# Optimization experiments

Measured on AMD Instinct MI355X. Metric: run time of the kernel, lower is better.

The kernel has to match this reference:

```python
import jax, jax.numpy as jnp
import numpy as np
from jax import lax

B, S, D, NH, K = 4, 2048, 1024, 16, 3
EPS = 1e-6


def custom_layernorm(x, gamma, beta):
    # torch-style: std with ddof=1, eps added to std (not var)
    mean = jnp.mean(x, axis=-1, keepdims=True)
    var = jnp.sum((x - mean) ** 2, axis=-1, keepdims=True) / (x.shape[-1] - 1)
    std = jnp.sqrt(var)
    return gamma * ((x - mean) / (std + EPS)) + beta


def setup_inputs() -> dict:
    key = jax.random.key(0)
    ks = jax.random.split(key, 10)
    s = 1.0 / np.sqrt(D)
    return {
        "x": jax.random.normal(ks[0], (B, S, D), jnp.float32),
        "Wq": jax.random.normal(ks[1], (D, D), jnp.float32) * s,
        "bq": jax.random.normal(ks[2], (D,), jnp.float32) * 0.02,
        "Wk": jax.random.normal(ks[3], (D, D), jnp.float32) * s,
        "Wv": jax.random.normal(ks[4], (D, D), jnp.float32) * s,
        "bv": jax.random.normal(ks[5], (D,), jnp.float32) * 0.02,
        "conv_w": jax.random.normal(ks[6], (D, D // NH, K), jnp.float32) * (1.0 / np.sqrt((D // NH) * K)),
        "conv_b": jax.random.normal(ks[7], (D,), jnp.float32) * 0.02,
        "gamma": jnp.ones((D,), jnp.float32),
        "beta": jnp.zeros((D,), jnp.float32),
        "Wo": jax.random.normal(ks[8], (D, D), jnp.float32) * s,
        "bo": jax.random.normal(ks[9], (D,), jnp.float32) * 0.02,
    }


def reference(x, Wq, bq, Wk, Wv, bv, conv_w, conv_b, gamma, beta, Wo, bo):
    d = x.shape[-1]
    groups = d // conv_w.shape[1]
    pad = conv_w.shape[2] // 2

    q = x @ Wq + bq
    k = x @ Wk  # key has no bias
    v = x @ Wv + bv

    # grouped conv1d over sequence dim (NCW layout)
    xc = jnp.transpose(x, (0, 2, 1))  # [B, D, S]
    conv_out = lax.conv_general_dilated(
        xc, conv_w, window_strides=(1,), padding=[(pad, pad)],
        feature_group_count=groups,
        dimension_numbers=("NCH", "OIH", "NCH"),
    ) + conv_b[None, :, None]
    conv_out = jnp.transpose(conv_out, (0, 2, 1))  # [B, S, D]
    conv_out = custom_layernorm(conv_out, gamma, beta)  # dropout = identity (eval)

    scale = 1.0 / jnp.sqrt(jnp.asarray(d, x.dtype))
    scores = jnp.einsum("bqd,bkd->bqk", q, k) * scale  # [B, S, S]
    attn = jax.nn.softmax(scores, axis=-1)
    attention_out = jnp.einsum("bqk,bkd->bqd", attn, v)

    combined = custom_layernorm(conv_out + attention_out, gamma, beta)
    return combined @ Wo + bo + x
```

## Files before the change

kernel.cpp:

```cpp
#include <hip/hip_runtime.h>
#include <cstdint>


#define DEV __device__ __forceinline__

typedef unsigned short u16;
typedef __attribute__((ext_vector_type(8))) short bf16x8;
typedef __attribute__((ext_vector_type(4))) float f32x4;

static const int Sn = 2048, Dn = 1024;

DEV float bf2f(u16 u) { union { unsigned int i; float f; } w; w.i = ((unsigned int)u) << 16; return w.f; }
DEV u16 f2bf(float f) {
  union { float f; unsigned int i; } w; w.f = f;
  unsigned int x = w.i;
  return (u16)((x + 0x7FFFu + ((x >> 16) & 1u)) >> 16);
}

DEV void gload_lds16(const u16* gsrc, u16* lds_dst) {
  __builtin_amdgcn_global_load_lds(
      (const __attribute__((address_space(1))) void*)gsrc,
      (__attribute__((address_space(3))) void*)lds_dst,
      16, 0, 0);
}

DEV float block_allreduce_sum(float v, float* red, int tid) {
  #pragma unroll
  for (int o = 32; o > 0; o >>= 1) v += __shfl_down(v, o, 64);
  __syncthreads();
  if ((tid & 63) == 0) red[tid >> 6] = v;
  __syncthreads();
  return red[0] + red[1] + red[2] + red[3];
}

DEV float block_allreduce_max(float v, float* red, int tid) {
  #pragma unroll
  for (int o = 32; o > 0; o >>= 1) v = fmaxf(v, __shfl_down(v, o, 64));
  __syncthreads();
  if ((tid & 63) == 0) red[tid >> 6] = v;
  __syncthreads();
  return fmaxf(fmaxf(red[0], red[1]), fmaxf(red[2], red[3]));
}

DEV void ln_row(const u16* __restrict__ a, const u16* __restrict__ b2,
                const float* __restrict__ gamma, const float* __restrict__ beta,
                u16* __restrict__ out, long row, int tid, float* red) {
  long base = row * Dn + tid * 4;
  ushort4 av = *(const ushort4*)&a[base];
  float v0 = bf2f(av.x), v1 = bf2f(av.y), v2 = bf2f(av.z), v3 = bf2f(av.w);
  if (b2) {
    ushort4 bv4 = *(const ushort4*)&b2[base];
    v0 += bf2f(bv4.x); v1 += bf2f(bv4.y); v2 += bf2f(bv4.z); v3 += bf2f(bv4.w);
  }
  float s = block_allreduce_sum(v0 + v1 + v2 + v3, red, tid);
  float mean = s * (1.0f / 1024.0f);
  float d0 = v0 - mean, d1 = v1 - mean, d2 = v2 - mean, d3 = v3 - mean;
  float sq = block_allreduce_sum(d0 * d0 + d1 * d1 + d2 * d2 + d3 * d3, red, tid);
  float inv = 1.0f / (sqrtf(sq * (1.0f / 1023.0f)) + 1e-6f);
  float4 gv = *(const float4*)&gamma[tid * 4];
  float4 bev = *(const float4*)&beta[tid * 4];
  ushort4 o;
  o.x = f2bf(gv.x * d0 * inv + bev.x);
  o.y = f2bf(gv.y * d1 * inv + bev.y);
  o.z = f2bf(gv.z * d2 * inv + bev.z);
  o.w = f2bf(gv.w * d3 * inv + bev.w);
  *(ushort4*)&out[base] = o;
}

__global__ __launch_bounds__(256)
void prep_all(const float* __restrict__ Wq, const float* __restrict__ Wk,
              const float* __restrict__ Wv, const float* __restrict__ Wo,
              u16* __restrict__ wT,
              const float* __restrict__ bq, const float* __restrict__ bv,
              float* __restrict__ qkvb,
              const float* __restrict__ x, u16* __restrict__ xb) {
  __shared__ u16 sm[64][68];
  int blk = blockIdx.x;
  int tid = threadIdx.x;
  if (blk < 1024) {
    int w = blk >> 8, t = blk & 255;
    const float* src = (w == 0) ? Wq : (w == 1) ? Wk : (w == 2) ? Wv : Wo;
    u16* dst = wT + (size_t)w * 1048576u;
    int i0 = (t >> 4) << 6, j0 = (t & 15) << 6;
    int tx = tid & 15, r0 = tid >> 4;
    #pragma unroll
    for (int rr = r0; rr < 64; rr += 16) {
      float4 v = *(const float4*)&src[(long)(i0 + rr) * 1024 + j0 + tx * 4];
      sm[rr][tx*4+0] = f2bf(v.x); sm[rr][tx*4+1] = f2bf(v.y);
      sm[rr][tx*4+2] = f2bf(v.z); sm[rr][tx*4+3] = f2bf(v.w);
    }
    __syncthreads();
    #pragma unroll
    for (int cc = r0; cc < 64; cc += 16) {
      ushort4 o;
      o.x = sm[tx*4+0][cc]; o.y = sm[tx*4+1][cc];
      o.z = sm[tx*4+2][cc]; o.w = sm[tx*4+3][cc];
      *(ushort4*)&dst[(long)(j0 + cc) * 1024 + i0 + tx * 4] = o;
    }
  } else if (blk == 1024) {
    for (int j = tid; j < 3072; j += 256) {
      float v = 0.0f;
      if (j < 1024) v = bq[j];
      else if (j >= 2048) v = bv[j - 2048];
      qkvb[j] = v;
    }
  } else {
    int i = (blk - 1025) * 1024 + tid * 4;
    float4 v = *(const float4*)&x[i];
    ushort4 o;
    o.x = f2bf(v.x); o.y = f2bf(v.y); o.z = f2bf(v.z); o.w = f2bf(v.w);
    *(ushort4*)&xb[i] = o;
  }
}

template<typename CT>
__global__ __launch_bounds__(256, 2)
void gemm_nt(const u16* __restrict__ A, const u16* __restrict__ A2, long Abs, int lda,
             const u16* __restrict__ B, long Bbs, int ldb,
             CT* __restrict__ C, CT* __restrict__ C2, long Cbs, int ldc,
             int zsplit, int K, float scale,
             const float* __restrict__ bias, int bias_bs,
             const float* __restrict__ res, long Rbs, int ldr) {
  __shared__ u16 sA[2][128 * 32];
  __shared__ u16 sB[2][128 * 32];
  int tid = threadIdx.x;
  int lane = tid & 63, wv = tid >> 6;
  int quad = lane >> 4, lm = lane & 15;
  int wr = wv >> 1, wc = wv & 1;
  long m0 = (long)blockIdx.x * 128, n0 = (long)blockIdx.y * 128;
  int z = blockIdx.z;
  if (z >= zsplit) { A = A2 + (long)(z - zsplit) * Abs; C = C2 + (long)(z - zsplit) * Cbs; }
  else             { A = A  + (long)z * Abs;            C = C  + (long)z * Cbs; }
  B += (long)z * Bbs;
  if (res) res += (long)z * Rbs;

  f32x4 acc[4][4] = {};

  int srow = wv * 16 + (lane >> 2);
  int sch = (lane & 3) * 8;
  const u16* Ap = A + (m0 + srow) * (long)lda + sch;
  const u16* Bp = B + (n0 + srow) * (long)ldb + sch;
  const int lofs = wv * 16 * 32;

  for (int k0 = 0; k0 < K; k0 += 64) {
    #pragma unroll
    for (int h = 0; h < 2; h++) {
      int kh = k0 + h * 32;
      gload_lds16(Ap + kh, &sA[h][lofs]);
      gload_lds16(Ap + 64 * (long)lda + kh, &sA[h][lofs + 64 * 32]);
      gload_lds16(Bp + kh, &sB[h][lofs]);
      gload_lds16(Bp + 64 * (long)ldb + kh, &sB[h][lofs + 64 * 32]);
    }
    __syncthreads();
    #pragma unroll
    for (int h = 0; h < 2; h++) {
      bf16x8 af[4], bfr[4];
      #pragma unroll
      for (int mi = 0; mi < 4; mi++)
        af[mi] = *(const bf16x8*)&sA[h][(wr * 64 + mi * 16 + lm) * 32 + quad * 8];
      #pragma unroll
      for (int ni = 0; ni < 4; ni++)
        bfr[ni] = *(const bf16x8*)&sB[h][(wc * 64 + ni * 16 + lm) * 32 + quad * 8];
      #pragma unroll
      for (int mi = 0; mi < 4; mi++)
        #pragma unroll
        for (int ni = 0; ni < 4; ni++)
          acc[mi][ni] = __builtin_amdgcn_mfma_f32_16x16x32_bf16(af[mi], bfr[ni], acc[mi][ni], 0, 0, 0);
    }
    __syncthreads();
  }

  #pragma unroll
  for (int mi = 0; mi < 4; mi++) {
    #pragma unroll
    for (int ni = 0; ni < 4; ni++) {
      int col = (int)n0 + wc * 64 + ni * 16 + lm;
      float bv = bias ? bias[(long)z * bias_bs + col] : 0.0f;
      #pragma unroll
      for (int r = 0; r < 4; r++) {
        long rowg = m0 + wr * 64 + mi * 16 + quad * 4 + r;
        float v = acc[mi][ni][r] * scale + bv;
        if (res) v += res[rowg * (long)ldr + col];
        if constexpr (sizeof(CT) == 2) C[rowg * (long)ldc + col] = f2bf(v);
        else                           C[rowg * (long)ldc + col] = v;
      }
    }
  }
}

__global__ __launch_bounds__(256, 2)
void post_qkv(int ngemm,
              const u16* __restrict__ Qb, const u16* __restrict__ Kb,
              u16* __restrict__ Pd, u16* __restrict__ Pw,
              const u16* __restrict__ Vb, u16* __restrict__ vt) {
  __shared__ u16 smem[2 * 2 * 128 * 32];
  int blk = blockIdx.x;
  int tid = threadIdx.x;
  if (blk < ngemm) {
    u16* sA0 = smem;
    u16* sB0 = smem + 2 * 128 * 32;
    int lane = tid & 63, wv = tid >> 6;
    int quad = lane >> 4, lm = lane & 15;
    int wr = wv >> 1, wc = wv & 1;
    int z = blk >> 8;
    long m0 = (long)(blk & 15) * 128, n0 = (long)((blk >> 4) & 15) * 128;
    const u16* A = Qb + (long)z * Sn * Dn;
    const u16* B = Kb + (long)z * Sn * Dn;
    u16* C = (z < 2) ? Pd + (long)z * Sn * Sn : Pw + (long)(z - 2) * Sn * Sn;

    f32x4 acc[4][4] = {};
    int srow = wv * 16 + (lane >> 2);
    int sch = (lane & 3) * 8;
    const u16* Ap = A + (m0 + srow) * 1024 + sch;
    const u16* Bp = B + (n0 + srow) * 1024 + sch;
    const int lofs = wv * 16 * 32;

    for (int k0 = 0; k0 < 1024; k0 += 64) {
      #pragma unroll
      for (int h = 0; h < 2; h++) {
        int kh = k0 + h * 32;
        gload_lds16(Ap + kh, &sA0[h * 128 * 32 + lofs]);
        gload_lds16(Ap + 64 * 1024 + kh, &sA0[h * 128 * 32 + lofs + 64 * 32]);
        gload_lds16(Bp + kh, &sB0[h * 128 * 32 + lofs]);
        gload_lds16(Bp + 64 * 1024 + kh, &sB0[h * 128 * 32 + lofs + 64 * 32]);
      }
      __syncthreads();
      #pragma unroll
      for (int h = 0; h < 2; h++) {
        bf16x8 af[4], bfr[4];
        #pragma unroll
        for (int mi = 0; mi < 4; mi++)
          af[mi] = *(const bf16x8*)&sA0[h * 128 * 32 + (wr * 64 + mi * 16 + lm) * 32 + quad * 8];
        #pragma unroll
        for (int ni = 0; ni < 4; ni++)
          bfr[ni] = *(const bf16x8*)&sB0[h * 128 * 32 + (wc * 64 + ni * 16 + lm) * 32 + quad * 8];
        #pragma unroll
        for (int mi = 0; mi < 4; mi++)
          #pragma unroll
          for (int ni = 0; ni < 4; ni++)
            acc[mi][ni] = __builtin_amdgcn_mfma_f32_16x16x32_bf16(af[mi], bfr[ni], acc[mi][ni], 0, 0, 0);
      }
      __syncthreads();
    }
    #pragma unroll
    for (int mi = 0; mi < 4; mi++) {
      #pragma unroll
      for (int ni = 0; ni < 4; ni++) {
        int col = (int)n0 + wc * 64 + ni * 16 + lm;
        #pragma unroll
        for (int r = 0; r < 4; r++) {
          long rowg = m0 + wr * 64 + mi * 16 + quad * 4 + r;
          C[rowg * 2048 + col] = f2bf(acc[mi][ni][r] * 0.03125f);
        }
      }
    }
  } else {
    u16 (*sm)[68] = (u16(*)[68])smem;
    int t = blk - ngemm;
    int b = t >> 9, r = t & 511;
    int j0 = (r & 15) << 6, i0 = ((r >> 4) & 31) << 6;
    const u16* s = Vb + (long)b * Sn * Dn;
    u16* d = vt + (long)b * Dn * Sn;
    int tx = tid & 15, r0 = tid >> 4;
    #pragma unroll
    for (int rr = r0; rr < 64; rr += 16) {
      ushort4 v = *(const ushort4*)&s[(long)(i0 + rr) * 1024 + j0 + tx * 4];
      sm[rr][tx*4+0] = v.x; sm[rr][tx*4+1] = v.y; sm[rr][tx*4+2] = v.z; sm[rr][tx*4+3] = v.w;
    }
    __syncthreads();
    #pragma unroll
    for (int cc = r0; cc < 64; cc += 16) {
      ushort4 o;
      o.x = sm[tx*4+0][cc]; o.y = sm[tx*4+1][cc];
      o.z = sm[tx*4+2][cc]; o.w = sm[tx*4+3][cc];
      *(ushort4*)&d[(long)(j0 + cc) * 2048 + i0 + tx * 4] = o;
    }
  }
}

__global__ __launch_bounds__(256)
void smax_conv(u16* __restrict__ pa, u16* __restrict__ pb, int rowsplit, int nsm,
               const float* __restrict__ x, const float* __restrict__ cw,
               const float* __restrict__ cb, u16* __restrict__ convo) {
  __shared__ u16 smem[22160];
  __shared__ float red[4];
  int blk = blockIdx.x;
  int tid = threadIdx.x;
  if (blk < nsm) {
    long row = blk;
    u16* p = (row < rowsplit) ? pa + row * 2048 : pb + (row - rowsplit) * 2048;
    ushort4 a = *(const ushort4*)&p[tid * 8];
    ushort4 b = *(const ushort4*)&p[tid * 8 + 4];
    float f0 = bf2f(a.x), f1 = bf2f(a.y), f2 = bf2f(a.z), f3 = bf2f(a.w);
    float f4 = bf2f(b.x), f5 = bf2f(b.y), f6 = bf2f(b.z), f7 = bf2f(b.w);
    float m = fmaxf(fmaxf(fmaxf(f0, f1), fmaxf(f2, f3)),
                    fmaxf(fmaxf(f4, f5), fmaxf(f6, f7)));
    m = block_allreduce_max(m, red, tid);
    float e0 = __expf(f0 - m), e1 = __expf(f1 - m), e2 = __expf(f2 - m), e3 = __expf(f3 - m);
    float e4 = __expf(f4 - m), e5 = __expf(f5 - m), e6 = __expf(f6 - m), e7 = __expf(f7 - m);
    float s = block_allreduce_sum(e0 + e1 + e2 + e3 + e4 + e5 + e6 + e7, red, tid);
    float inv = 1.0f / s;
    ushort4 o1, o2;
    o1.x = f2bf(e0 * inv); o1.y = f2bf(e1 * inv); o1.z = f2bf(e2 * inv); o1.w = f2bf(e3 * inv);
    o2.x = f2bf(e4 * inv); o2.y = f2bf(e5 * inv); o2.z = f2bf(e6 * inv); o2.w = f2bf(e7 * inv);
    *(ushort4*)&p[tid * 8] = o1;
    *(ushort4*)&p[tid * 8 + 4] = o2;
  } else {
    u16 (*sx)[72] = (u16(*)[72])smem;
    u16 (*sw)[200] = (u16(*)[200])(smem + 9360);
    int r = blk - nsm;
    int s0 = (r & 15) * 128;
    int g = (r >> 4) & 15;
    int b = r >> 8;
    int lane = tid & 63, wv = tid >> 6;
    int quad = lane >> 4, lm = lane & 15;
    for (int idx = tid; idx < 64 * 192; idx += 256) {
      int oc = idx / 192, k = idx - oc * 192;
      int t = k >> 6, i = k & 63;
      sw[oc][k] = f2bf(cw[((long)(g * 64 + oc)) * 192 + i * 3 + t]);
    }
    for (int idx = tid; idx < 130 * 16; idx += 256) {
      int rr = idx >> 4, c4 = (idx & 15) * 4;
      int s = s0 - 1 + rr;
      ushort4 v;
      if (s >= 0 && s < Sn) {
        float4 f = *(const float4*)&x[((long)b * Sn + s) * Dn + g * 64 + c4];
        v.x = f2bf(f.x); v.y = f2bf(f.y); v.z = f2bf(f.z); v.w = f2bf(f.w);
      } else { v.x = 0; v.y = 0; v.z = 0; v.w = 0; }
      *(ushort4*)&sx[rr][c4] = v;
    }
    __syncthreads();
    f32x4 acc[2][4] = {};
    #pragma unroll
    for (int ks = 0; ks < 6; ks++) {
      int t = ks >> 1;
      int i0 = (ks & 1) * 32 + quad * 8;
      bf16x8 a0 = *(const bf16x8*)&sx[wv * 32 + lm + t][i0];
      bf16x8 a1 = *(const bf16x8*)&sx[wv * 32 + 16 + lm + t][i0];
      #pragma unroll
      for (int nf = 0; nf < 4; nf++) {
        bf16x8 bf = *(const bf16x8*)&sw[nf * 16 + lm][ks * 32 + quad * 8];
        acc[0][nf] = __builtin_amdgcn_mfma_f32_16x16x32_bf16(a0, bf, acc[0][nf], 0, 0, 0);
        acc[1][nf] = __builtin_amdgcn_mfma_f32_16x16x32_bf16(a1, bf, acc[1][nf], 0, 0, 0);
      }
    }
    #pragma unroll
    for (int mi = 0; mi < 2; mi++) {
      #pragma unroll
      for (int nf = 0; nf < 4; nf++) {
        int col = g * 64 + nf * 16 + lm;
        float bias = cb[col];
        #pragma unroll
        for (int rr = 0; rr < 4; rr++) {
          int row = wv * 32 + mi * 16 + quad * 4 + rr;
          convo[((long)b * Sn + s0 + row) * Dn + col] = f2bf(acc[mi][nf][rr] + bias);
        }
      }
    }
  }
}

__global__ __launch_bounds__(256, 2)
void pv_ln(int npv,
           const u16* __restrict__ Pd, const u16* __restrict__ Pw,
           const u16* __restrict__ vt, u16* __restrict__ attn,
           u16* __restrict__ conv,
           const float* __restrict__ gamma, const float* __restrict__ beta) {
  __shared__ u16 smem[2 * 2 * 128 * 32];
  __shared__ float red[4];
  int blk = blockIdx.x;
  int tid = threadIdx.x;
  if (blk < npv) {
    u16* sA0 = smem;
    u16* sB0 = smem + 2 * 128 * 32;
    int lane = tid & 63, wv = tid >> 6;
    int quad = lane >> 4, lm = lane & 15;
    int wr = wv >> 1, wc = wv & 1;
    int z = blk >> 7;
    long m0 = (long)(blk & 15) * 128, n0 = (long)((blk >> 4) & 7) * 128;
    const u16* A = (z < 2) ? Pd + (long)z * Sn * Sn : Pw + (long)(z - 2) * Sn * Sn;
    const u16* B = vt + (long)z * Dn * Sn;
    u16* C = attn + (long)z * Sn * Dn;

    f32x4 acc[4][4] = {};
    int srow = wv * 16 + (lane >> 2);
    int sch = (lane & 3) * 8;
    const u16* Ap = A + (m0 + srow) * 2048 + sch;
    const u16* Bp = B + (n0 + srow) * 2048 + sch;
    const int lofs = wv * 16 * 32;

    for (int k0 = 0; k0 < 2048; k0 += 64) {
      #pragma unroll
      for (int h = 0; h < 2; h++) {
        int kh = k0 + h * 32;
        gload_lds16(Ap + kh, &sA0[h * 128 * 32 + lofs]);
        gload_lds16(Ap + 64 * 2048 + kh, &sA0[h * 128 * 32 + lofs + 64 * 32]);
        gload_lds16(Bp + kh, &sB0[h * 128 * 32 + lofs]);
        gload_lds16(Bp + 64 * 2048 + kh, &sB0[h * 128 * 32 + lofs + 64 * 32]);
      }
      __syncthreads();
      #pragma unroll
      for (int h = 0; h < 2; h++) {
        bf16x8 af[4], bfr[4];
        #pragma unroll
        for (int mi = 0; mi < 4; mi++)
          af[mi] = *(const bf16x8*)&sA0[h * 128 * 32 + (wr * 64 + mi * 16 + lm) * 32 + quad * 8];
        #pragma unroll
        for (int ni = 0; ni < 4; ni++)
          bfr[ni] = *(const bf16x8*)&sB0[h * 128 * 32 + (wc * 64 + ni * 16 + lm) * 32 + quad * 8];
        #pragma unroll
        for (int mi = 0; mi < 4; mi++)
          #pragma unroll
          for (int ni = 0; ni < 4; ni++)
            acc[mi][ni] = __builtin_amdgcn_mfma_f32_16x16x32_bf16(af[mi], bfr[ni], acc[mi][ni], 0, 0, 0);
      }
      __syncthreads();
    }
    #pragma unroll
    for (int mi = 0; mi < 4; mi++) {
      #pragma unroll
      for (int ni = 0; ni < 4; ni++) {
        int col = (int)n0 + wc * 64 + ni * 16 + lm;
        #pragma unroll
        for (int r = 0; r < 4; r++) {
          long rowg = m0 + wr * 64 + mi * 16 + quad * 4 + r;
          C[rowg * 1024 + col] = f2bf(acc[mi][ni][r]);
        }
      }
    }
  } else {
    long row = blk - npv;
    ln_row(conv, nullptr, gamma, beta, conv, row, tid, red);
  }
}

__global__ __launch_bounds__(256)
void ln_kernel(const u16* __restrict__ a, const u16* __restrict__ b2,
               const float* __restrict__ gamma, const float* __restrict__ beta,
               u16* __restrict__ out) {
  __shared__ float red[4];
  ln_row(a, b2, gamma, beta, out, blockIdx.x, threadIdx.x, red);
}

static const size_t OFF_WT    = 0;
static const size_t OFF_QKVB  = 8ull << 20;
static const size_t OFF_Q     = 9ull << 20;
static const size_t OFF_K     = 25ull << 20;
static const size_t OFF_V     = 41ull << 20;
static const size_t OFF_PW    = 57ull << 20;

extern "C" void kernel_launch(void* const* d_in, const int* in_sizes, int n_in,
                              void* d_out, int out_size, void* d_ws, size_t ws_size,
                              hipStream_t stream) {
  const float* x     = (const float*)d_in[0];
  const float* Wq    = (const float*)d_in[1];
  const float* bq    = (const float*)d_in[2];
  const float* Wk    = (const float*)d_in[3];
  const float* Wv    = (const float*)d_in[4];
  const float* bv    = (const float*)d_in[5];
  const float* cw    = (const float*)d_in[6];
  const float* cb    = (const float*)d_in[7];
  const float* gamma = (const float*)d_in[8];
  const float* beta  = (const float*)d_in[9];
  const float* Wo    = (const float*)d_in[10];
  const float* bo    = (const float*)d_in[11];
  float* out = (float*)d_out;
  char* ws = (char*)d_ws;

  u16*   wT    = (u16*)(ws + OFF_WT);
  float* qkvb  = (float*)(ws + OFF_QKVB);
  u16*   Qb    = (u16*)(ws + OFF_Q);
  u16*   Kb    = (u16*)(ws + OFF_K);
  u16*   Vb    = (u16*)(ws + OFF_V);
  u16*   Pw    = (u16*)(ws + OFF_PW);
  u16*   xb    = (u16*)d_out;
  u16*   Pd    = (u16*)d_out;
  u16*   vt    = (u16*)d_out + 8388608;
  u16*   conv  = Vb;
  u16*   attn  = Qb;
  u16*   combined = Kb;
  const long PBS = (long)Sn * Sn;

  dim3 tb(256);

  prep_all<<<dim3(9217), tb, 0, stream>>>(Wq, Wk, Wv, Wo, wT, bq, bv, qkvb, x, xb);
  gemm_nt<u16><<<dim3(64, 8, 3), tb, 0, stream>>>(
      xb, nullptr, 0, 1024, wT, 1048576, 1024, Qb, (u16*)nullptr, 8388608, 1024,
      99, 1024, 1.0f, qkvb, 1024, nullptr, 0, 0);

  if (ws_size >= (73ull << 20)) {
    post_qkv<<<dim3(1024 + 2048), tb, 0, stream>>>(1024, Qb, Kb, Pd, Pw, Vb, vt);
    smax_conv<<<dim3(8192 + 1024), tb, 0, stream>>>(Pd, Pw, 4096, 8192,
                                                    x, cw, cb, conv);
    pv_ln<<<dim3(512 + 8192), tb, 0, stream>>>(512, Pd, Pw, vt, attn, conv,
                                               gamma, beta);
  } else {
    post_qkv<<<dim3(2048), tb, 0, stream>>>(0, Qb, Kb, Pd, Pw, Vb, vt);
    for (int c = 0; c < 2; c++) {
      long off = (long)c * 2 * Sn * Dn;
      gemm_nt<u16><<<dim3(16, 16, 2), tb, 0, stream>>>(
          Qb + off, nullptr, (long)Sn * Dn, 1024, Kb + off, (long)Sn * Dn, 1024,
          Pd, (u16*)nullptr, PBS, 2048,
          99, 1024, 0.03125f, nullptr, 0, nullptr, 0, 0);
      smax_conv<<<dim3(4096 + (c == 0 ? 1024 : 0)), tb, 0, stream>>>(
          Pd, Pd, 4096, 4096, x, cw, cb, conv);
      gemm_nt<u16><<<dim3(16, 8, 2), tb, 0, stream>>>(
          Pd, nullptr, PBS, 2048, vt + off, (long)Dn * Sn, 2048,
          attn + off, (u16*)nullptr, (long)Sn * Dn, 1024,
          99, 2048, 1.0f, nullptr, 0, nullptr, 0, 0);
    }
    ln_kernel<<<dim3(8192), tb, 0, stream>>>(conv, nullptr, gamma, beta, conv);
  }

  ln_kernel<<<dim3(8192), tb, 0, stream>>>(conv, attn, gamma, beta, combined);
  gemm_nt<float><<<dim3(64, 8, 1), tb, 0, stream>>>(
      combined, nullptr, 0, 1024, wT + 3u * 1048576u, 0, 1024,
      out, (float*)nullptr, 0, 1024,
      99, 1024, 1.0f, bo, 0, x, 0, 1024);
}
```

Baseline: 354.0 us.

## Add 256x256 eight-wave GEMM for QKV and QK^T, fold V transpose into softmax

Adds a new 512-thread GEMM kernel with 256x256 tiles, 128KB dynamic LDS double buffering, swizzled direct-to-LDS loads and interleaved barrier/setprio scheduling. It is used for the QKV projection and, in the large-workspace path, for the QK^T score GEMM, which replaces post_qkv. The V transpose moves into extra blocks of the softmax/conv kernel, and conv output is relocated to Kb. The larger tiles are meant to improve data reuse and MFMA utilisation, at the cost of lower occupancy and fewer blocks per launch.

```diff
diff --git a/kernel.cpp b/kernel.cpp
--- a/kernel.cpp
+++ b/kernel.cpp
@@ -111,6 +111,161 @@
     o.x = f2bf(v.x); o.y = f2bf(v.y); o.z = f2bf(v.z); o.w = f2bf(v.w);
     *(ushort4*)&xb[i] = o;
   }
+}
+
+__global__ __launch_bounds__(512, 2)
+void gemm8(const u16* __restrict__ A, long Abs, int lda,
+           const u16* __restrict__ B, long Bbs, int ldb,
+           u16* __restrict__ C0, u16* __restrict__ C1, int zsplit,
+           long Cbs, int ldc, int K, float scale,
+           const float* __restrict__ bias, int bias_bs) {
+  extern __shared__ u16 lds[];
+  int tid = threadIdx.x;
+  int w = tid >> 6, ln = tid & 63;
+  int quad = ln >> 4, lm = ln & 15;
+  int wr = w >> 2, wc = w & 3;
+  long m0 = (long)blockIdx.x * 256, n0 = (long)blockIdx.y * 256;
+  int z = blockIdx.z;
+  A += (long)z * Abs;
+  B += (long)z * Bbs;
+  u16* C = (z < zsplit) ? C0 + (long)z * Cbs : C1 + (long)(z - zsplit) * Cbs;
+
+  int sg = ((ln & 7) ^ (ln >> 3)) * 8;
+  int row0 = w * 8 + (ln >> 3);
+  const u16* As0 = A + (m0 + row0) * (long)lda + sg;
+  const u16* As1 = As0 + 64 * (long)lda;
+  const u16* Bs0 = B + (n0 + row0) * (long)ldb + sg;
+  const u16* Bs1 = Bs0 + 64 * (long)ldb;
+  u16* dA = lds + w * 512;
+  u16* dB = lds + 16384 + w * 512;
+
+  int rA = wr * 16 + lm;
+  int rB = wc * 16 + lm;
+  int g0 = (quad ^ (lm & 7)) * 8;
+  int g1 = ((4 + quad) ^ (lm & 7)) * 8;
+
+#define STGA(buf, h, k0) do { \
+    gload_lds16(As0 + (long)(h) * 128 * lda + (k0), dA + (buf) * 32768 + (h) * 8192); \
+    gload_lds16(As1 + (long)(h) * 128 * lda + (k0), dA + (buf) * 32768 + (h) * 8192 + 4096); } while (0)
+#define STGB(buf, h, k0) do { \
+    gload_lds16(Bs0 + (long)(h) * 128 * ldb + (k0), dB + (buf) * 32768 + (h) * 8192); \
+    gload_lds16(Bs1 + (long)(h) * 128 * ldb + (k0), dB + (buf) * 32768 + (h) * 8192 + 4096); } while (0)
+#define LDA_F(ab, mi, kk) (*(const bf16x8*)&lds[(ab) + ((mi) * 32 + rA) * 64 + ((kk) ? g1 : g0)])
+#define LDB_F(bb, ni, kk) (*(const bf16x8*)&lds[(bb) + ((ni) * 64 + rB) * 64 + ((kk) ? g1 : g0)])
+#define MFMA(a, b, c) __builtin_amdgcn_mfma_f32_16x16x32_bf16(a, b, c, 0, 0, 0)
+
+  f32x4 acc[8][4] = {};
+  bf16x8 bfr[4][2];
+  int nt = K >> 6;
+
+  STGB(0, 0, 0); STGB(0, 1, 0); STGA(0, 0, 0); STGA(0, 1, 0);
+  asm volatile("s_waitcnt vmcnt(2)" ::: "memory");
+  __builtin_amdgcn_sched_barrier(0);
+  __builtin_amdgcn_s_barrier();
+
+  for (int t = 0; t < nt; ++t) {
+    int buf = t & 1;
+    int abase = buf * 32768, bbase = abase + 16384;
+    int nbuf = buf ^ 1;
+    int kn = (t + 1) << 6;
+    bool more = (t + 1 < nt);
+
+    {
+      #pragma unroll
+      for (int ni = 0; ni < 4; ni++) {
+        bfr[ni][0] = LDB_F(bbase, ni, 0);
+        bfr[ni][1] = LDB_F(bbase, ni, 1);
+      }
+      bf16x8 a00 = LDA_F(abase, 0, 0), a01 = LDA_F(abase, 0, 1);
+      bf16x8 a10 = LDA_F(abase, 1, 0), a11 = LDA_F(abase, 1, 1);
+      if (more) STGB(nbuf, 0, kn);
+      __builtin_amdgcn_s_barrier();
+      __builtin_amdgcn_s_setprio(1);
+      #pragma unroll
+      for (int ni = 0; ni < 4; ni++) {
+        acc[0][ni] = MFMA(a00, bfr[ni][0], acc[0][ni]);
+        acc[0][ni] = MFMA(a01, bfr[ni][1], acc[0][ni]);
+        acc[1][ni] = MFMA(a10, bfr[ni][0], acc[1][ni]);
+        acc[1][ni] = MFMA(a11, bfr[ni][1], acc[1][ni]);
+      }
+      __builtin_amdgcn_s_setprio(0);
+      __builtin_amdgcn_s_barrier();
+    }
+    {
+      bf16x8 a00 = LDA_F(abase, 2, 0), a01 = LDA_F(abase, 2, 1);
+      bf16x8 a10 = LDA_F(abase, 3, 0), a11 = LDA_F(abase, 3, 1);
+      if (more) STGB(nbuf, 1, kn);
+      __builtin_amdgcn_s_barrier();
+      __builtin_amdgcn_s_setprio(1);
+      #pragma unroll
+      for (int ni = 0; ni < 4; ni++) {
+        acc[2][ni] = MFMA(a00, bfr[ni][0], acc[2][ni]);
+        acc[2][ni] = MFMA(a01, bfr[ni][1], acc[2][ni]);
+        acc[3][ni] = MFMA(a10, bfr[ni][0], acc[3][ni]);
+        acc[3][ni] = MFMA(a11, bfr[ni][1], acc[3][ni]);
+      }
+      __builtin_amdgcn_s_setprio(0);
+      if (more) asm volatile("s_waitcnt vmcnt(4)" ::: "memory");
+      else      asm volatile("s_waitcnt vmcnt(0)" ::: "memory");
+      __builtin_amdgcn_sched_barrier(0);
+      __builtin_amdgcn_s_barrier();
+    }
+    {
+      bf16x8 a00 = LDA_F(abase, 4, 0), a01 = LDA_F(abase, 4, 1);
+      bf16x8 a10 = LDA_F(abase, 5, 0), a11 = LDA_F(abase, 5, 1);
+      if (more) STGA(nbuf, 0, kn);
+      __builtin_amdgcn_s_barrier();
+      __builtin_amdgcn_s_setprio(1);
+      #pragma unroll
+      for (int ni = 0; ni < 4; ni++) {
+        acc[4][ni] = MFMA(a00, bfr[ni][0], acc[4][ni]);
+        acc[4][ni] = MFMA(a01, bfr[ni][1], acc[4][ni]);
+        acc[5][ni] = MFMA(a10, bfr[ni][0], acc[5][ni]);
+        acc[5][ni] = MFMA(a11, bfr[ni][1], acc[5][ni]);
+      }
+      __builtin_amdgcn_s_setprio(0);
+      __builtin_amdgcn_s_barrier();
+    }
+    {
+      bf16x8 a00 = LDA_F(abase, 6, 0), a01 = LDA_F(abase, 6, 1);
+      bf16x8 a10 = LDA_F(abase, 7, 0), a11 = LDA_F(abase, 7, 1);
+      if (more) STGA(nbuf, 1, kn);
+      __builtin_amdgcn_s_barrier();
+      __builtin_amdgcn_s_setprio(1);
+      #pragma unroll
+      for (int ni = 0; ni < 4; ni++) {
+        acc[6][ni] = MFMA(a00, bfr[ni][0], acc[6][ni]);
+        acc[6][ni] = MFMA(a01, bfr[ni][1], acc[6][ni]);
+        acc[7][ni] = MFMA(a10, bfr[ni][0], acc[7][ni]);
+        acc[7][ni] = MFMA(a11, bfr[ni][1], acc[7][ni]);
+      }
+      __builtin_amdgcn_s_setprio(0);
+      if (more) {
+        asm volatile("s_waitcnt vmcnt(2)" ::: "memory");
+        __builtin_amdgcn_sched_barrier(0);
+      }
+      __builtin_amdgcn_s_barrier();
+    }
+  }
+
+  #pragma unroll
+  for (int mi = 0; mi < 8; mi++) {
+    #pragma unroll
+    for (int ni = 0; ni < 4; ni++) {
+      int col = (int)n0 + ni * 64 + wc * 16 + lm;
+      float bvv = bias ? bias[(long)z * bias_bs + col] : 0.0f;
+      #pragma unroll
+      for (int r = 0; r < 4; r++) {
+        long rowg = m0 + mi * 32 + wr * 16 + quad * 4 + r;
+        C[rowg * (long)ldc + col] = f2bf(acc[mi][ni][r] * scale + bvv);
+      }
+    }
+  }
+#undef STGA
+#undef STGB
+#undef LDA_F
+#undef LDB_F
+#undef MFMA
 }
 
 template<typename CT>
@@ -279,9 +434,11 @@
 }
 
 __global__ __launch_bounds__(256)
-void smax_conv(u16* __restrict__ pa, u16* __restrict__ pb, int rowsplit, int nsm,
+void smax_conv(u16* __restrict__ pa, u16* __restrict__ pb, int rowsplit,
+               int nsm, int nconv,
                const float* __restrict__ x, const float* __restrict__ cw,
-               const float* __restrict__ cb, u16* __restrict__ convo) {
+               const float* __restrict__ cb, u16* __restrict__ convo,
+               const u16* __restrict__ Vb, u16* __restrict__ vt) {
   __shared__ u16 smem[22160];
   __shared__ float red[4];
   int blk = blockIdx.x;
@@ -305,7 +462,7 @@
     o2.x = f2bf(e4 * inv); o2.y = f2bf(e5 * inv); o2.z = f2bf(e6 * inv); o2.w = f2bf(e7 * inv);
     *(ushort4*)&p[tid * 8] = o1;
     *(ushort4*)&p[tid * 8 + 4] = o2;
-  } else {
+  } else if (blk < nsm + nconv) {
     u16 (*sx)[72] = (u16(*)[72])smem;
     u16 (*sw)[200] = (u16(*)[200])(smem + 9360);
     int r = blk - nsm;
@@ -356,6 +513,27 @@
           convo[((long)b * Sn + s0 + row) * Dn + col] = f2bf(acc[mi][nf][rr] + bias);
         }
       }
+    }
+  } else {
+    u16 (*sm)[68] = (u16(*)[68])smem;
+    int t = blk - nsm - nconv;
+    int b = t >> 9, r = t & 511;
+    int j0 = (r & 15) << 6, i0 = ((r >> 4) & 31) << 6;
+    const u16* s = Vb + (long)b * Sn * Dn;
+    u16* d = vt + (long)b * Dn * Sn;
+    int tx = tid & 15, r0 = tid >> 4;
+    #pragma unroll
+    for (int rr = r0; rr < 64; rr += 16) {
+      ushort4 v = *(const ushort4*)&s[(long)(i0 + rr) * 1024 + j0 + tx * 4];
+      sm[rr][tx*4+0] = v.x; sm[rr][tx*4+1] = v.y; sm[rr][tx*4+2] = v.z; sm[rr][tx*4+3] = v.w;
+    }
+    __syncthreads();
+    #pragma unroll
+    for (int cc = r0; cc < 64; cc += 16) {
+      ushort4 o;
+      o.x = sm[tx*4+0][cc]; o.y = sm[tx*4+1][cc];
+      o.z = sm[tx*4+2][cc]; o.w = sm[tx*4+3][cc];
+      *(ushort4*)&d[(long)(j0 + cc) * 2048 + i0 + tx * 4] = o;
     }
   }
 }
@@ -476,25 +654,39 @@
   u16*   xb    = (u16*)d_out;
   u16*   Pd    = (u16*)d_out;
   u16*   vt    = (u16*)d_out + 8388608;
-  u16*   conv  = Vb;
   u16*   attn  = Qb;
   u16*   combined = Kb;
   const long PBS = (long)Sn * Sn;
 
+  static int gemm8_attr = 0;
+  if (!gemm8_attr) {
+    hipFuncSetAttribute((const void*)gemm8,
+                        hipFuncAttributeMaxDynamicSharedMemorySize, 131072);
+    gemm8_attr = 1;
+  }
+
   dim3 tb(256);
+  dim3 tb8(512);
 
   prep_all<<<dim3(9217), tb, 0, stream>>>(Wq, Wk, Wv, Wo, wT, bq, bv, qkvb, x, xb);
-  gemm_nt<u16><<<dim3(64, 8, 3), tb, 0, stream>>>(
-      xb, nullptr, 0, 1024, wT, 1048576, 1024, Qb, (u16*)nullptr, 8388608, 1024,
-      99, 1024, 1.0f, qkvb, 1024, nullptr, 0, 0);
+  gemm8<<<dim3(32, 4, 3), tb8, 131072, stream>>>(
+      xb, 0, 1024, wT, 1048576, 1024,
+      Qb, (u16*)nullptr, 99, 8388608, 1024,
+      1024, 1.0f, qkvb, 1024);
 
   if (ws_size >= (73ull << 20)) {
-    post_qkv<<<dim3(1024 + 2048), tb, 0, stream>>>(1024, Qb, Kb, Pd, Pw, Vb, vt);
-    smax_conv<<<dim3(8192 + 1024), tb, 0, stream>>>(Pd, Pw, 4096, 8192,
-                                                    x, cw, cb, conv);
+    u16* conv = Kb;
+    gemm8<<<dim3(8, 8, 4), tb8, 131072, stream>>>(
+        Qb, (long)Sn * Dn, 1024, Kb, (long)Sn * Dn, 1024,
+        Pd, Pw, 2, PBS, 2048,
+        1024, 0.03125f, nullptr, 0);
+    smax_conv<<<dim3(8192 + 1024 + 2048), tb, 0, stream>>>(
+        Pd, Pw, 4096, 8192, 1024, x, cw, cb, conv, Vb, vt);
     pv_ln<<<dim3(512 + 8192), tb, 0, stream>>>(512, Pd, Pw, vt, attn, conv,
                                                gamma, beta);
+    ln_kernel<<<dim3(8192), tb, 0, stream>>>(conv, attn, gamma, beta, combined);
   } else {
+    u16* conv = Vb;
     post_qkv<<<dim3(2048), tb, 0, stream>>>(0, Qb, Kb, Pd, Pw, Vb, vt);
     for (int c = 0; c < 2; c++) {
       long off = (long)c * 2 * Sn * Dn;
@@ -503,16 +695,16 @@
           Pd, (u16*)nullptr, PBS, 2048,
           99, 1024, 0.03125f, nullptr, 0, nullptr, 0, 0);
       smax_conv<<<dim3(4096 + (c == 0 ? 1024 : 0)), tb, 0, stream>>>(
-          Pd, Pd, 4096, 4096, x, cw, cb, conv);
+          Pd, Pd, 4096, 4096, (c == 0 ? 1024 : 0), x, cw, cb, conv, Vb, vt);
       gemm_nt<u16><<<dim3(16, 8, 2), tb, 0, stream>>>(
           Pd, nullptr, PBS, 2048, vt + off, (long)Dn * Sn, 2048,
           attn + off, (u16*)nullptr, (long)Sn * Dn, 1024,
           99, 2048, 1.0f, nullptr, 0, nullptr, 0, 0);
     }
     ln_kernel<<<dim3(8192), tb, 0, stream>>>(conv, nullptr, gamma, beta, conv);
-  }
-
-  ln_kernel<<<dim3(8192), tb, 0, stream>>>(conv, attn, gamma, beta, combined);
+    ln_kernel<<<dim3(8192), tb, 0, stream>>>(conv, attn, gamma, beta, combined);
+  }
+
   gemm_nt<float><<<dim3(64, 8, 1), tb, 0, stream>>>(
       combined, nullptr, 0, 1024, wT + 3u * 1048576u, 0, 1024,
       out, (float*)nullptr, 0, 1024,
```

Measured after the change: 365.0 us. 1.03x slower.
